# Kernel tuning notes

Measured on AMD Instinct MI355X. Metric: run time of the kernel, lower is better.

## Reference

```python
import jax, jax.numpy as jnp
import numpy as np

N = 50000   # nodes
E = 1600000 # edges
G = 256     # graphs
EPS = 1e-5  # batchnorm eps (torch default)


def _bn(h, g, b):
    # training-mode BatchNorm1d: biased batch stats
    m = h.mean(0)
    v = h.var(0)
    return (h - m) * jax.lax.rsqrt(v + EPS) * g + b


def _mlp(h, W1, b1, g, be, W2, b2):
    # Lin -> BN -> ReLU -> Lin
    h = jax.nn.relu(_bn(h @ W1 + b1, g, be))
    return h @ W2 + b2


def _scatter_mean(v, idx, n):
    s = jax.ops.segment_sum(v, idx, num_segments=n)
    c = jax.ops.segment_sum(jnp.ones((v.shape[0], 1), v.dtype), idx, num_segments=n)
    return s / jnp.maximum(c, 1.0)


def setup_inputs() -> dict:
    key = jax.random.key(0)
    ks = iter(jax.random.split(key, 32))
    d = {}
    d["x"] = jax.random.normal(next(ks), (N, 48), dtype=jnp.float32)
    d["edge_index"] = jax.random.randint(next(ks), (2, E), 0, N, dtype=jnp.int64)
    d["batch"] = jnp.sort(jax.random.randint(next(ks), (N,), 0, G, dtype=jnp.int64))

    def lin(k, fin, fout):
        kw, kb = jax.random.split(k)
        s = 1.0 / np.sqrt(fin)
        return (jax.random.uniform(kw, (fin, fout), jnp.float32, -s, s),
                jax.random.uniform(kb, (fout,), jnp.float32, -s, s))

    # input BatchNorm1d(48)
    d["bn_g"] = jnp.ones((48,), jnp.float32)
    d["bn_b"] = jnp.zeros((48,), jnp.float32)

    def mlp_params(prefix, fin, fmid, fout):
        W1, b1 = lin(next(ks), fin, fmid)
        W2, b2 = lin(next(ks), fmid, fout)
        d[prefix + "_W1"], d[prefix + "_b1"] = W1, b1
        d[prefix + "_g"] = jnp.ones((fmid,), jnp.float32)
        d[prefix + "_be"] = jnp.zeros((fmid,), jnp.float32)
        d[prefix + "_W2"], d[prefix + "_b2"] = W2, b2

    mlp_params("e", 96, 128, 128)    # EdgeBlock
    mlp_params("n1", 176, 128, 128)  # NodeBlock mlp1
    mlp_params("n2", 176, 128, 128)  # NodeBlock mlp2
    mlp_params("gl", 128, 128, 2)    # GlobalBlock
    return d


def reference(x, edge_index, batch, bn_g, bn_b,
              e_W1, e_b1, e_g, e_be, e_W2, e_b2,
              n1_W1, n1_b1, n1_g, n1_be, n1_W2, n1_b2,
              n2_W1, n2_b1, n2_g, n2_be, n2_W2, n2_b2,
              gl_W1, gl_b1, gl_g, gl_be, gl_W2, gl_b2):
    x = _bn(x, bn_g, bn_b)
    row, col = edge_index[0], edge_index[1]
    # EdgeBlock: cat(src, dest) -> MLP
    edge_attr = _mlp(jnp.concatenate([x[row], x[col]], axis=1),
                     e_W1, e_b1, e_g, e_be, e_W2, e_b2)
    # NodeBlock: cat(x[row], edge_attr) -> mlp1 -> scatter_mean(col) -> cat(x,.) -> mlp2
    m = _mlp(jnp.concatenate([x[row], edge_attr], axis=1),
             n1_W1, n1_b1, n1_g, n1_be, n1_W2, n1_b2)
    agg = _scatter_mean(m, col, N)
    x2 = _mlp(jnp.concatenate([x, agg], axis=1),
              n2_W1, n2_b1, n2_g, n2_be, n2_W2, n2_b2)
    # GlobalBlock: scatter_mean over graphs -> MLP -> [G, 2]
    u = _scatter_mean(x2, batch, G)
    u = _mlp(u, gl_W1, gl_b1, gl_g, gl_be, gl_W2, gl_b2)
    return u
```

## Files before the change

kernel.cpp:

```cpp
#include <hip/hip_runtime.h>
#include <hip/hip_bf16.h>
#include <stdint.h>

#define DEV static __device__ __forceinline__

constexpr int N_ = 50000;
constexpr int E_ = 1600000;
constexpr int G_ = 256;

typedef __attribute__((ext_vector_type(8))) short short8;
typedef __attribute__((ext_vector_type(4))) float float4v;

DEV uint16_t f2bf(float f){
  uint32_t u = __float_as_uint(f);
  uint32_t r = (u + 0x7fffu + ((u >> 16) & 1u)) >> 16;
  return (uint16_t)r;
}
DEV void unpack2(uint32_t p, float& a, float& b){
  a = __uint_as_float(p << 16);
  b = __uint_as_float(p & 0xffff0000u);
}
DEV uint32_t pack2(float a, float b){
  return (uint32_t)f2bf(a) | ((uint32_t)f2bf(b) << 16);
}

__global__ __launch_bounds__(256) void k_xstats(const float* __restrict__ x, float* __restrict__ xstats){
  __shared__ float lst[96];
  int t = threadIdx.x;
  if (t < 96) lst[t] = 0.f;
  __syncthreads();
  int gid = blockIdx.x * 256 + t;
  int c4 = (gid % 12) * 4;
  float s[4] = {0,0,0,0}, q[4] = {0,0,0,0};
  const float4v* x4 = (const float4v*)x;
  for (int i = gid; i < N_ * 12; i += 64512){
    float4v v = x4[i];
    #pragma unroll
    for (int j = 0; j < 4; j++){ s[j] += v[j]; q[j] += v[j]*v[j]; }
  }
  #pragma unroll
  for (int j = 0; j < 4; j++){
    atomicAdd(&lst[c4 + j], s[j]);
    atomicAdd(&lst[48 + c4 + j], q[j]);
  }
  __syncthreads();
  if (t < 96) atomicAdd(&xstats[t], lst[t]);
}

__global__ void k_xfin(const float* __restrict__ xstats, const float* __restrict__ g,
                       const float* __restrict__ b, float* __restrict__ sx, float* __restrict__ tx){
  int c = threadIdx.x;
  if (c < 48){
    float m = xstats[c] / (float)N_;
    float v = xstats[48 + c] / (float)N_ - m*m;
    float s = g[c] / sqrtf(v + 1e-5f);
    sx[c] = s; tx[c] = b[c] - m*s;
  }
}

__global__ __launch_bounds__(256) void k_hist(const int* __restrict__ ei, int* __restrict__ counts){
  int e = blockIdx.x * 256 + threadIdx.x;
  if (e < E_) atomicAdd(&counts[ei[E_ + e]], 1);
}

__global__ __launch_bounds__(256) void k_invc(const int* __restrict__ counts, float* __restrict__ invc){
  int n = blockIdx.x * 256 + threadIdx.x;
  if (n < N_){ int c = counts[n]; invc[n] = (c > 0) ? 1.f/(float)c : 0.f; }
}

__global__ __launch_bounds__(256) void k_scan(const int* __restrict__ counts, int* __restrict__ off, int* __restrict__ cur){
  __shared__ int wsum[4];
  __shared__ int carry_s;
  int t = threadIdx.x, lane = t & 63, w = t >> 6;
  if (t == 0) carry_s = 0;
  __syncthreads();
  for (int base = 0; base < N_; base += 1024){
    int i0 = base + t * 4;
    int v0 = (i0 + 0 < N_) ? counts[i0 + 0] : 0;
    int v1 = (i0 + 1 < N_) ? counts[i0 + 1] : 0;
    int v2 = (i0 + 2 < N_) ? counts[i0 + 2] : 0;
    int v3 = (i0 + 3 < N_) ? counts[i0 + 3] : 0;
    int tsum = v0 + v1 + v2 + v3;
    int xs = tsum;
    for (int d = 1; d < 64; d <<= 1){ int y = __shfl_up(xs, d); if (lane >= d) xs += y; }
    if (lane == 63) wsum[w] = xs;
    __syncthreads();
    int woff = 0;
    for (int k = 0; k < w; k++) woff += wsum[k];
    int excl = xs - tsum + woff + carry_s;
    int e0 = excl, e1 = e0 + v0, e2 = e1 + v1, e3 = e2 + v2;
    if (i0 + 0 < N_){ off[i0+0] = e0; cur[i0+0] = e0; }
    if (i0 + 1 < N_){ off[i0+1] = e1; cur[i0+1] = e1; }
    if (i0 + 2 < N_){ off[i0+2] = e2; cur[i0+2] = e2; }
    if (i0 + 3 < N_){ off[i0+3] = e3; cur[i0+3] = e3; }
    __syncthreads();
    if (t == 0) carry_s += wsum[0] + wsum[1] + wsum[2] + wsum[3];
    __syncthreads();
  }
  if (t == 0) off[N_] = carry_s;
}

__global__ __launch_bounds__(256) void k_place(const int* __restrict__ ei, int* __restrict__ cur,
                                               int2* __restrict__ rcs){
  int e = blockIdx.x * 256 + threadIdx.x;
  if (e < E_){
    int c = ei[E_ + e];
    int p = atomicAdd(&cur[c], 1);
    rcs[p] = make_int2(ei[e], c);
  }
}

__global__ __launch_bounds__(256) void k_wprep(
    const float* __restrict__ eW2, const float* __restrict__ n1W1,
    const float* __restrict__ n1W2, const float* __restrict__ n2W1,
    const float* __restrict__ n2W2, const float* __restrict__ glW1,
    const float* __restrict__ n1b2, const float* __restrict__ n2b2,
    uint16_t* __restrict__ Mt, float* __restrict__ Wcomb,
    float* __restrict__ M3, float* __restrict__ c1, float* __restrict__ c3){
  int flat = blockIdx.x * 256 + threadIdx.x;
  if (flat < 16384){
    int n = flat & 127, k = flat >> 7;
    float a = 0.f;
    for (int j = 0; j < 128; j++) a += eW2[k*128 + j] * n1W1[(48 + j)*128 + n];
    Mt[n*128 + k] = f2bf(a);
  } else if (flat < 32768){
    int b = flat - 16384;
    int n = b & 127, j = b >> 7;
    float a = 0.f;
    for (int m = 0; m < 128; m++) a += n1W2[j*128 + m] * n2W1[(48 + m)*128 + n];
    Wcomb[(48 + j)*128 + n] = a;
  } else if (flat < 38912){
    int b = flat - 32768;
    int n = b & 127, k = b >> 7;
    Wcomb[k*128 + n] = n2W1[k*128 + n];
  } else if (flat < 55296){
    int b = flat - 38912;
    int n = b & 127, j = b >> 7;
    float a = 0.f;
    for (int m = 0; m < 128; m++) a += n2W2[j*128 + m] * glW1[m*128 + n];
    M3[j*128 + n] = a;
  } else if (flat < 55552){
    int e = flat - 55296;
    if (e < 128){
      float a = 0.f;
      for (int m = 0; m < 128; m++) a += n1b2[m] * n2W1[(48 + m)*128 + e];
      c1[e] = a;
    } else {
      int n = e - 128;
      float a = 0.f;
      for (int m = 0; m < 128; m++) a += n2b2[m] * glW1[m*128 + n];
      c3[n] = a;
    }
  }
}

__global__ __launch_bounds__(256) void k_nodegemm(
    const float* __restrict__ x, const float* __restrict__ sx, const float* __restrict__ tx,
    const float* __restrict__ eW1, const float* __restrict__ n1W1,
    uint16_t* __restrict__ AC, uint16_t* __restrict__ Bn){
  __shared__ float xT[48][36];
  __shared__ float W[48][128];
  int t = threadIdx.x;
  int n0 = blockIdx.x * 32;
  for (int idx = t; idx < 384; idx += 256){
    int r = idx / 12, q = idx % 12;
    int n = n0 + r;
    float4v v = {0.f,0.f,0.f,0.f};
    if (n < N_) v = *(const float4v*)&x[(size_t)n*48 + q*4];
    #pragma unroll
    for (int i = 0; i < 4; i++){
      int k = q*4 + i;
      xT[k][r] = v[i] * sx[k] + tx[k];
    }
  }
  int cg = t & 31, ng = t >> 5;
  const float* Wsrc0 = eW1;
  const float* Wsrc1 = eW1 + 48*128;
  const float* Wsrc2 = n1W1;
  for (int seg = 0; seg < 3; seg++){
    const float* Wsrc = (seg == 0) ? Wsrc0 : (seg == 1) ? Wsrc1 : Wsrc2;
    __syncthreads();
    {
      const float4v* src4 = (const float4v*)Wsrc;
      float4v* W4 = (float4v*)W;
      for (int idx = t; idx < 1536; idx += 256) W4[idx] = src4[idx];
    }
    __syncthreads();
    float acc[4][4] = {{0.f}};
    #pragma unroll 4
    for (int k = 0; k < 48; k++){
      float4v xv = *(const float4v*)&xT[k][ng*4];
      float4v wv = *(const float4v*)&W[k][cg*4];
      #pragma unroll
      for (int i = 0; i < 4; i++)
        #pragma unroll
        for (int j = 0; j < 4; j++)
          acc[i][j] += xv[i]*wv[j];
    }
    #pragma unroll
    for (int i = 0; i < 4; i++){
      int n = n0 + ng*4 + i;
      if (n >= N_) continue;
      uint2 pv;
      pv.x = pack2(acc[i][0], acc[i][1]);
      pv.y = pack2(acc[i][2], acc[i][3]);
      if (seg == 0)      *(uint2*)&AC[(size_t)n*256 + cg*4] = pv;
      else if (seg == 1) *(uint2*)&Bn[(size_t)n*128 + cg*4] = pv;
      else               *(uint2*)&AC[(size_t)n*256 + 128 + cg*4] = pv;
    }
  }
}

__global__ __launch_bounds__(256) void k_estats(const int2* __restrict__ rcs,
    const uint16_t* __restrict__ AC, const uint16_t* __restrict__ Bn, float* __restrict__ estR){
  __shared__ float red[4][64][4];
  __shared__ float lst[256];
  int t = threadIdx.x, lane = t & 63, w = t >> 6;
  int wid = blockIdx.x * 4 + w, nw = gridDim.x * 4;
  float s0=0,q0=0,s1=0,q1=0;
  const uint32_t* ACu = (const uint32_t*)AC;
  const uint32_t* Bu  = (const uint32_t*)Bn;
  for (int e = wid; e < E_; e += nw){
    int2 rc = rcs[e];
    uint32_t pa = ACu[(size_t)rc.x*128 + lane];
    uint32_t pb = Bu[(size_t)rc.y*64 + lane];
    float a0,a1,b0,b1; unpack2(pa,a0,a1); unpack2(pb,b0,b1);
    float h0 = a0 + b0, h1 = a1 + b1;
    s0 += h0; q0 += h0*h0; s1 += h1; q1 += h1*h1;
  }
  red[w][lane][0]=s0; red[w][lane][1]=q0; red[w][lane][2]=s1; red[w][lane][3]=q1;
  __syncthreads();
  if (t < 64){
    float S0=0,Q0=0,S1=0,Q1=0;
    for (int ww = 0; ww < 4; ww++){ S0+=red[ww][t][0]; Q0+=red[ww][t][1]; S1+=red[ww][t][2]; Q1+=red[ww][t][3]; }
    lst[2*t] = S0; lst[2*t+1] = S1; lst[128+2*t] = Q0; lst[128+2*t+1] = Q1;
  }
  __syncthreads();
  atomicAdd(&estR[(blockIdx.x & 63)*256 + t], lst[t]);
}

__global__ void k_bnfin(const float* __restrict__ statsR, int reps, const float* __restrict__ g,
                        const float* __restrict__ be, float* __restrict__ s_out, float* __restrict__ t_out,
                        float inv_n){
  int c = threadIdx.x;
  if (c >= 128) return;
  float sm = 0.f, sq = 0.f;
  for (int r = 0; r < reps; r++){ sm += statsR[r*256 + c]; sq += statsR[r*256 + 128 + c]; }
  float m = sm * inv_n;
  float v = sq * inv_n - m*m;
  float s = g[c] / sqrtf(v + 1e-5f);
  s_out[c] = s;
  t_out[c] = be[c] - m*s;
}

__global__ __launch_bounds__(256) void k_epass(
    const int2* __restrict__ rcs,
    const uint16_t* __restrict__ AC, const uint16_t* __restrict__ Bn,
    const uint16_t* __restrict__ Mt, const float* __restrict__ se, const float* __restrict__ te,
    const float* __restrict__ sn1, const float* __restrict__ tn1,
    int mode, float* __restrict__ n1R, float* __restrict__ aggf){
  __shared__ __align__(16) uint16_t bufA[64*136];
  __shared__ __align__(16) uint16_t bufB[128*136];
  __shared__ float sete[512];
  __shared__ float lst[256];
  __shared__ int srow[64], scol[64], ssid[64], scolseg[64];
  __shared__ int snseg;
  const int t = threadIdx.x;
  const long i0 = (long)blockIdx.x * 64;
  const int lane = t & 63, w = t >> 6;
  const int m = lane & 15, quad = lane >> 4;

  if (t < 128){ sete[t] = se[t]; sete[128 + t] = te[t]; sete[256 + t] = sn1[t]; sete[384 + t] = tn1[t]; }
  if (mode == 0) lst[t] = 0.f;
  if (t < 64){ int2 rc = rcs[i0 + t]; srow[t] = rc.x; scol[t] = rc.y; }
  __syncthreads();

  if (mode == 1 && t < 64){
    bool bnd = (t > 0) && (scol[t] != scol[t-1]);
    unsigned long long mask = __ballot(bnd);
    int sid = __popcll(mask << (63 - t));
    ssid[t] = sid;
    if (bnd || t == 0) scolseg[sid] = scol[t];
    if (t == 63) snseg = sid + 1;
  }

  {
    int e = t >> 2, q = t & 3;
    int r = srow[e], c = scol[e];
    const uint4* Ap = (const uint4*)((const uint32_t*)AC + (size_t)r*128 + q*16);
    const uint4* Bp = (const uint4*)((const uint32_t*)Bn + (size_t)c*64  + q*16);
    uint4* dst = (uint4*)((uint32_t*)bufA + e*68 + q*16);
    int cb = q*32;
    #pragma unroll
    for (int u = 0; u < 4; u++){
      uint4 va = Ap[u], vb = Bp[u];
      float4v sA = *(const float4v*)&sete[cb + u*8];
      float4v sB = *(const float4v*)&sete[cb + u*8 + 4];
      float4v tA = *(const float4v*)&sete[128 + cb + u*8];
      float4v tB = *(const float4v*)&sete[128 + cb + u*8 + 4];
      float a0,a1,b0,b1; uint4 o;
      unpack2(va.x,a0,a1); unpack2(vb.x,b0,b1);
      o.x = pack2(fmaxf(0.f,(a0+b0)*sA[0]+tA[0]), fmaxf(0.f,(a1+b1)*sA[1]+tA[1]));
      unpack2(va.y,a0,a1); unpack2(vb.y,b0,b1);
      o.y = pack2(fmaxf(0.f,(a0+b0)*sA[2]+tA[2]), fmaxf(0.f,(a1+b1)*sA[3]+tA[3]));
      unpack2(va.z,a0,a1); unpack2(vb.z,b0,b1);
      o.z = pack2(fmaxf(0.f,(a0+b0)*sB[0]+tB[0]), fmaxf(0.f,(a1+b1)*sB[1]+tB[1]));
      unpack2(va.w,a0,a1); unpack2(vb.w,b0,b1);
      o.w = pack2(fmaxf(0.f,(a0+b0)*sB[2]+tB[2]), fmaxf(0.f,(a1+b1)*sB[3]+tB[3]));
      dst[u] = o;
    }
  }
  {
    int n = t >> 1, h = t & 1;
    const uint4* src = (const uint4*)((const uint32_t*)Mt + n*64 + h*32);
    uint4* dst = (uint4*)((uint32_t*)bufB + n*68 + h*32);
    #pragma unroll
    for (int u = 0; u < 8; u++) dst[u] = src[u];
  }
  __syncthreads();

  float4v acc[8];
  #pragma unroll
  for (int nt = 0; nt < 8; nt++){ acc[nt][0]=0.f; acc[nt][1]=0.f; acc[nt][2]=0.f; acc[nt][3]=0.f; }
  {
    const uint16_t* aptr = bufA + (w*16 + m)*136 + quad*8;
    const uint16_t* bbase = bufB + m*136 + quad*8;
    #pragma unroll
    for (int ks = 0; ks < 4; ks++){
      short8 af = *(const short8*)(aptr + ks*32);
      #pragma unroll
      for (int nt = 0; nt < 8; nt++){
        short8 bf = *(const short8*)(bbase + nt*16*136 + ks*32);
        acc[nt] = __builtin_amdgcn_mfma_f32_16x16x32_bf16(af, bf, acc[nt], 0, 0, 0);
      }
    }
  }
  __syncthreads();

  {
    int e = t >> 2, q = t & 3;
    int r = srow[e];
    const uint4* src = (const uint4*)((const uint32_t*)AC + (size_t)r*128 + 64 + q*16);
    uint4* dst = (uint4*)((uint32_t*)bufA + e*68 + q*16);
    #pragma unroll
    for (int u = 0; u < 4; u++) dst[u] = src[u];
  }
  #pragma unroll
  for (int nt = 0; nt < 8; nt++)
    #pragma unroll
    for (int reg = 0; reg < 4; reg++)
      bufB[(w*16 + quad*4 + reg)*136 + nt*16 + m] = f2bf(acc[nt][reg]);
  if (mode == 1 && snseg <= 32){
    float* segacc = (float*)(bufB + 8704);
    for (int i = t; i < snseg*128; i += 256) segacc[i] = 0.f;
  }
  __syncthreads();

  if (mode == 0){
    int cp = t & 63, eg = t >> 6;
    float ss0=0,qq0=0,ss1=0,qq1=0;
    #pragma unroll
    for (int it = 0; it < 16; it++){
      int e = eg*16 + it;
      uint32_t ph = ((uint32_t*)bufB)[e*68 + cp];
      uint32_t pc = ((uint32_t*)bufA)[e*68 + cp];
      float h0,h1,c0,c1v;
      unpack2(ph,h0,h1); unpack2(pc,c0,c1v);
      float v0 = h0 + c0, v1 = h1 + c1v;
      ss0 += v0; qq0 += v0*v0; ss1 += v1; qq1 += v1*v1;
    }
    atomicAdd(&lst[2*cp], ss0);
    atomicAdd(&lst[2*cp+1], ss1);
    atomicAdd(&lst[128+2*cp], qq0);
    atomicAdd(&lst[128+2*cp+1], qq1);
    __syncthreads();
    atomicAdd(&n1R[(blockIdx.x & 63)*256 + t], lst[t]);
  } else {
    int cp = t & 63, eg = t >> 6;
    float s0 = sete[256+2*cp], s1 = sete[256+2*cp+1];
    float b0 = sete[384+2*cp], b1 = sete[384+2*cp+1];
    int nseg = snseg;
    bool lp = (nseg <= 32);
    float* segacc = (float*)(bufB + 8704);
    int cursid = ssid[eg*16];
    float r0 = 0.f, r1 = 0.f;
    for (int it = 0; it < 16; it++){
      int e = eg*16 + it;
      uint32_t ph = ((uint32_t*)bufB)[e*68 + cp];
      uint32_t pc = ((uint32_t*)bufA)[e*68 + cp];
      float h0,h1,c0,c1v;
      unpack2(ph,h0,h1); unpack2(pc,c0,c1v);
      float v0 = fmaxf(0.f, (h0+c0)*s0 + b0);
      float v1 = fmaxf(0.f, (h1+c1v)*s1 + b1);
      int sid = ssid[e];
      if (sid != cursid){
        if (lp){ atomicAdd(&segacc[cursid*128 + 2*cp], r0); atomicAdd(&segacc[cursid*128 + 2*cp+1], r1); }
        else { int c = scolseg[cursid];
               atomicAdd(&aggf[(size_t)c*128 + 2*cp], r0); atomicAdd(&aggf[(size_t)c*128 + 2*cp+1], r1); }
        cursid = sid; r0 = 0.f; r1 = 0.f;
      }
      r0 += v0; r1 += v1;
    }
    if (lp){ atomicAdd(&segacc[cursid*128 + 2*cp], r0); atomicAdd(&segacc[cursid*128 + 2*cp+1], r1); }
    else { int c = scolseg[cursid];
           atomicAdd(&aggf[(size_t)c*128 + 2*cp], r0); atomicAdd(&aggf[(size_t)c*128 + 2*cp+1], r1); }
    __syncthreads();
    if (lp){
      for (int idx = t; idx < nseg*64; idx += 256){
        int s = idx >> 6, cpp = idx & 63;
        float v0 = segacc[s*128 + 2*cpp], v1 = segacc[s*128 + 2*cpp+1];
        int c = scolseg[s];
        float* dst = &aggf[(size_t)c*128 + 2*cpp];
        if (s == 0 || s == nseg - 1){ atomicAdd(dst, v0); atomicAdd(dst+1, v1); }
        else { dst[0] = v0; dst[1] = v1; }
      }
    }
  }
}

__global__ __launch_bounds__(256) void k_n2(const float* __restrict__ x,
    const float* __restrict__ sx, const float* __restrict__ tx,
    const float* __restrict__ aggf, const float* __restrict__ invc,
    const float* __restrict__ Wc, const float* __restrict__ c1, const int* __restrict__ counts,
    float* __restrict__ hn2, float* __restrict__ n2R){
  __shared__ float xT[44][36];
  __shared__ float wT[44][128];
  __shared__ float lst[256];
  int t = threadIdx.x;
  int n0 = blockIdx.x * 32;
  int cg = t & 31, ng = t >> 5;
  lst[t] = 0.f;
  float acc[4][4] = {{0.f}};
  for (int kc = 0; kc < 176; kc += 44){
    __syncthreads();
    for (int idx = t; idx < 32*44; idx += 256){
      int r = idx / 44, k = idx % 44;
      int n = n0 + r, kk = kc + k;
      float v = 0.f;
      if (n < N_){
        if (kk < 48) v = x[(size_t)n*48 + kk] * sx[kk] + tx[kk];
        else         v = aggf[(size_t)n*128 + (kk - 48)] * invc[n];
      }
      xT[k][r] = v;
    }
    for (int idx = t; idx < 44*128; idx += 256){
      int k = idx >> 7, c = idx & 127;
      wT[k][c] = Wc[(kc + k)*128 + c];
    }
    __syncthreads();
    for (int k = 0; k < 44; k++){
      float4v xv = *(const float4v*)&xT[k][ng*4];
      float4v wv = *(const float4v*)&wT[k][cg*4];
      #pragma unroll
      for (int i = 0; i < 4; i++)
        #pragma unroll
        for (int j = 0; j < 4; j++)
          acc[i][j] += xv[i]*wv[j];
    }
  }
  float csum[4] = {0,0,0,0}, cqs[4] = {0,0,0,0};
  for (int i = 0; i < 4; i++){
    int n = n0 + ng*4 + i;
    if (n >= N_) continue;
    bool ok = counts[n] > 0;
    float4v o;
    #pragma unroll
    for (int j = 0; j < 4; j++){
      float vv = acc[i][j] + (ok ? c1[cg*4 + j] : 0.f);
      o[j] = vv; csum[j] += vv; cqs[j] += vv*vv;
    }
    *(float4v*)&hn2[(size_t)n*128 + cg*4] = o;
  }
  #pragma unroll
  for (int j = 0; j < 4; j++){
    atomicAdd(&lst[cg*4 + j], csum[j]);
    atomicAdd(&lst[128 + cg*4 + j], cqs[j]);
  }
  __syncthreads();
  atomicAdd(&n2R[(blockIdx.x & 63)*256 + t], lst[t]);
}

__global__ void k_goff(const int* __restrict__ batch, int* __restrict__ goff){
  int g = threadIdx.x;
  int lo = 0, hi = N_;
  while (lo < hi){ int mid = (lo + hi) >> 1; if (batch[mid] < g) lo = mid + 1; else hi = mid; }
  goff[g] = lo;
  if (g == 0) goff[256] = N_;
}

__global__ __launch_bounds__(128) void k_gmean(const float* __restrict__ hn2, const int* __restrict__ goff,
    const float* __restrict__ sn2, const float* __restrict__ tn2, float* __restrict__ gmean){
  int g = blockIdx.x, c = threadIdx.x;
  int b = goff[g], e = goff[g+1];
  float s = sn2[c], tt = tn2[c], a = 0.f;
  for (int r = b; r < e; r++) a += fmaxf(0.f, hn2[(size_t)r*128 + c]*s + tt);
  gmean[g*128 + c] = (e > b) ? a/(float)(e - b) : 0.f;
}

__global__ __launch_bounds__(256) void k_hg(const float* __restrict__ gmean, const float* __restrict__ M3,
    const float* __restrict__ c3, const int* __restrict__ goff,
    float* __restrict__ hg, float* __restrict__ gls){
  int idx = blockIdx.x * 256 + threadIdx.x;
  int g = idx >> 7, c = idx & 127;
  float a = 0.f;
  for (int k = 0; k < 128; k++) a += gmean[g*128 + k] * M3[k*128 + c];
  if (goff[g+1] > goff[g]) a += c3[c];
  hg[idx] = a;
  atomicAdd(&gls[c], a);
  atomicAdd(&gls[128 + c], a*a);
}

__global__ __launch_bounds__(256) void k_out(const float* __restrict__ hg, const float* __restrict__ sgl,
    const float* __restrict__ tgl, const float* __restrict__ glW2, const float* __restrict__ glb2,
    float* __restrict__ out){
  int idx = blockIdx.x * 256 + threadIdx.x;
  int g = idx >> 1, o = idx & 1;
  float a = 0.f;
  for (int c = 0; c < 128; c++){
    float r = fmaxf(0.f, hg[g*128 + c]*sgl[c] + tgl[c]);
    a += r * glW2[c*2 + o];
  }
  out[idx] = a + glb2[o];
}

extern "C" void kernel_launch(void* const* d_in, const int* in_sizes, int n_in,
                              void* d_out, int out_size, void* d_ws, size_t ws_size,
                              hipStream_t stream){
  const float* x     = (const float*)d_in[0];
  const int*   ei    = (const int*)d_in[1];
  const int*   batch = (const int*)d_in[2];
  const float* bn_g  = (const float*)d_in[3];
  const float* bn_b  = (const float*)d_in[4];
  const float* eW1   = (const float*)d_in[5];
  const float* e_g   = (const float*)d_in[7];
  const float* e_be  = (const float*)d_in[8];
  const float* eW2   = (const float*)d_in[9];
  const float* n1W1  = (const float*)d_in[11];
  const float* n1_g  = (const float*)d_in[13];
  const float* n1_be = (const float*)d_in[14];
  const float* n1W2  = (const float*)d_in[15];
  const float* n1b2  = (const float*)d_in[16];
  const float* n2W1  = (const float*)d_in[17];
  const float* n2_g  = (const float*)d_in[19];
  const float* n2_be = (const float*)d_in[20];
  const float* n2W2  = (const float*)d_in[21];
  const float* n2b2  = (const float*)d_in[22];
  const float* glW1  = (const float*)d_in[23];
  const float* gl_g  = (const float*)d_in[25];
  const float* gl_be = (const float*)d_in[26];
  const float* glW2  = (const float*)d_in[27];
  const float* glb2  = (const float*)d_in[28];
  float* out = (float*)d_out;

  char* w = (char*)d_ws;
  size_t off = 0;
  auto take = [&](size_t bytes) -> char* {
    char* p = w + off;
    off = (off + bytes + 511) & ~(size_t)511;
    return p;
  };

  const size_t ZONE_WORDS = 96 + 3*64*256 + 256 + N_;
  float* zone   = (float*)take(ZONE_WORDS * 4);
  float* xstats = zone;
  float* estR   = zone + 96;
  float* n1R    = zone + 96 + 64*256;
  float* n2R    = zone + 96 + 2*64*256;
  float* gls    = zone + 96 + 3*64*256;
  int*   counts = (int*)(zone + 96 + 3*64*256 + 256);

  float* sx = (float*)take(48*4);   float* tx = (float*)take(48*4);
  float* se = (float*)take(128*4);  float* te = (float*)take(128*4);
  float* sn1 = (float*)take(128*4); float* tn1 = (float*)take(128*4);
  float* sn2 = (float*)take(128*4); float* tn2 = (float*)take(128*4);
  float* sgl = (float*)take(128*4); float* tgl = (float*)take(128*4);
  float* c1 = (float*)take(128*4);  float* c3 = (float*)take(128*4);
  float* invc  = (float*)take((size_t)N_*4);
  float* Wcomb = (float*)take(176*128*4);
  float* M3    = (float*)take(128*128*4);
  float* gmean = (float*)take(G_*128*4);
  float* hg    = (float*)take(G_*128*4);
  int* offs = (int*)take((N_+1)*4);
  int* cur  = (int*)take(N_*4);
  int* goff = (int*)take(257*4);
  uint16_t* Mt = (uint16_t*)take(128*128*2);
  uint16_t* AC = (uint16_t*)take((size_t)N_*256*2);
  uint16_t* Bn = (uint16_t*)take((size_t)N_*128*2);
  float* aggf  = (float*)take((size_t)N_*128*4);
  float* hn2   = (float*)take((size_t)N_*128*4);
  int2* rcs = (int2*)take((size_t)E_*8);

  if (off > ws_size) return;

  hipMemsetAsync(zone, 0, ZONE_WORDS*4, stream);
  hipMemsetAsync(aggf, 0, (size_t)N_*128*4, stream);

  hipLaunchKernelGGL(k_xstats, dim3(252), dim3(256), 0, stream, x, xstats);
  hipLaunchKernelGGL(k_hist, dim3((E_+255)/256), dim3(256), 0, stream, ei, counts);
  hipLaunchKernelGGL(k_xfin, dim3(1), dim3(64), 0, stream, xstats, bn_g, bn_b, sx, tx);
  hipLaunchKernelGGL(k_scan, dim3(1), dim3(256), 0, stream, counts, offs, cur);
  hipLaunchKernelGGL(k_place, dim3((E_+255)/256), dim3(256), 0, stream, ei, cur, rcs);
  hipLaunchKernelGGL(k_invc, dim3((N_+255)/256), dim3(256), 0, stream, counts, invc);
  hipLaunchKernelGGL(k_wprep, dim3(217), dim3(256), 0, stream,
                     eW2, n1W1, n1W2, n2W1, n2W2, glW1, n1b2, n2b2, Mt, Wcomb, M3, c1, c3);
  hipLaunchKernelGGL(k_nodegemm, dim3((N_+31)/32), dim3(256), 0, stream,
                     x, sx, tx, eW1, n1W1, AC, Bn);
  hipLaunchKernelGGL(k_estats, dim3(1024), dim3(256), 0, stream, rcs, AC, Bn, estR);
  hipLaunchKernelGGL(k_bnfin, dim3(1), dim3(128), 0, stream, estR, 64, e_g, e_be, se, te, 1.f/(float)E_);
  hipLaunchKernelGGL(k_epass, dim3(E_/64), dim3(256), 0, stream,
                     rcs, AC, Bn, Mt, se, te, se, te, 0, n1R, aggf);
  hipLaunchKernelGGL(k_bnfin, dim3(1), dim3(128), 0, stream, n1R, 64, n1_g, n1_be, sn1, tn1, 1.f/(float)E_);
  hipLaunchKernelGGL(k_epass, dim3(E_/64), dim3(256), 0, stream,
                     rcs, AC, Bn, Mt, se, te, sn1, tn1, 1, n1R, aggf);
  hipLaunchKernelGGL(k_n2, dim3((N_+31)/32), dim3(256), 0, stream,
                     x, sx, tx, aggf, invc, Wcomb, c1, counts, hn2, n2R);
  hipLaunchKernelGGL(k_bnfin, dim3(1), dim3(128), 0, stream, n2R, 64, n2_g, n2_be, sn2, tn2, 1.f/(float)N_);
  hipLaunchKernelGGL(k_goff, dim3(1), dim3(256), 0, stream, batch, goff);
  hipLaunchKernelGGL(k_gmean, dim3(256), dim3(128), 0, stream, hn2, goff, sn2, tn2, gmean);
  hipLaunchKernelGGL(k_hg, dim3(128), dim3(256), 0, stream, gmean, M3, c3, goff, hg, gls);
  hipLaunchKernelGGL(k_bnfin, dim3(1), dim3(128), 0, stream, gls, 1, gl_g, gl_be, sgl, tgl, 1.f/(float)G_);
  hipLaunchKernelGGL(k_out, dim3(2), dim3(256), 0, stream, hg, sgl, tgl, glW2, glb2, out);
}
```

Baseline: 1.691 ms.

## Split edge pass into stats and aggregate kernels with smaller LDS footprint

Replaces the mode-switched edge-pass kernel with two specialised kernels. The stats kernel computes BN sums straight from MFMA accumulators with wave shuffles, so it no longer writes the bf16 hidden tile back to LDS. Both kernels shrink the LDS row pitch from 136 to 132 and pack segment and scale scratch into the B buffer, cutting shared memory per block to fit more blocks per CU. The trade-off is a smaller segment-accumulator limit (24 instead of 32), which sends more blocks to global atomics, plus a changed bank-conflict pattern from the new padding.

```diff
diff --git a/kernel.cpp b/kernel.cpp
--- a/kernel.cpp
+++ b/kernel.cpp
@@ -16,6 +16,7 @@
   uint32_t r = (u + 0x7fffu + ((u >> 16) & 1u)) >> 16;
   return (uint16_t)r;
 }
+DEV float bf2f(uint16_t v){ return __uint_as_float((uint32_t)v << 16); }
 DEV void unpack2(uint32_t p, float& a, float& b){
   a = __uint_as_float(p << 16);
   b = __uint_as_float(p & 0xffff0000u);
@@ -253,43 +254,32 @@
   t_out[c] = be[c] - m*s;
 }
 
-__global__ __launch_bounds__(256) void k_epass(
+__global__ __launch_bounds__(256) void k_epass0(
     const int2* __restrict__ rcs,
     const uint16_t* __restrict__ AC, const uint16_t* __restrict__ Bn,
     const uint16_t* __restrict__ Mt, const float* __restrict__ se, const float* __restrict__ te,
-    const float* __restrict__ sn1, const float* __restrict__ tn1,
-    int mode, float* __restrict__ n1R, float* __restrict__ aggf){
-  __shared__ __align__(16) uint16_t bufA[64*136];
-  __shared__ __align__(16) uint16_t bufB[128*136];
-  __shared__ float sete[512];
+    float* __restrict__ n1R){
+  __shared__ __align__(16) uint16_t bufA[64*132];
+  __shared__ __align__(16) uint16_t bufB[128*132];
+  __shared__ float sete[256];
   __shared__ float lst[256];
-  __shared__ int srow[64], scol[64], ssid[64], scolseg[64];
-  __shared__ int snseg;
+  __shared__ int srow[64], scol[64];
   const int t = threadIdx.x;
   const long i0 = (long)blockIdx.x * 64;
   const int lane = t & 63, w = t >> 6;
   const int m = lane & 15, quad = lane >> 4;
 
-  if (t < 128){ sete[t] = se[t]; sete[128 + t] = te[t]; sete[256 + t] = sn1[t]; sete[384 + t] = tn1[t]; }
-  if (mode == 0) lst[t] = 0.f;
+  if (t < 128){ sete[t] = se[t]; sete[128 + t] = te[t]; }
+  lst[t] = 0.f;
   if (t < 64){ int2 rc = rcs[i0 + t]; srow[t] = rc.x; scol[t] = rc.y; }
   __syncthreads();
-
-  if (mode == 1 && t < 64){
-    bool bnd = (t > 0) && (scol[t] != scol[t-1]);
-    unsigned long long mask = __ballot(bnd);
-    int sid = __popcll(mask << (63 - t));
-    ssid[t] = sid;
-    if (bnd || t == 0) scolseg[sid] = scol[t];
-    if (t == 63) snseg = sid + 1;
-  }
 
   {
     int e = t >> 2, q = t & 3;
     int r = srow[e], c = scol[e];
     const uint4* Ap = (const uint4*)((const uint32_t*)AC + (size_t)r*128 + q*16);
     const uint4* Bp = (const uint4*)((const uint32_t*)Bn + (size_t)c*64  + q*16);
-    uint4* dst = (uint4*)((uint32_t*)bufA + e*68 + q*16);
+    uint4* dst = (uint4*)((uint32_t*)bufA + e*66 + q*16);
     int cb = q*32;
     #pragma unroll
     for (int u = 0; u < 4; u++){
@@ -313,7 +303,7 @@
   {
     int n = t >> 1, h = t & 1;
     const uint4* src = (const uint4*)((const uint32_t*)Mt + n*64 + h*32);
-    uint4* dst = (uint4*)((uint32_t*)bufB + n*68 + h*32);
+    uint4* dst = (uint4*)((uint32_t*)bufB + n*66 + h*32);
     #pragma unroll
     for (int u = 0; u < 8; u++) dst[u] = src[u];
   }
@@ -323,14 +313,14 @@
   #pragma unroll
   for (int nt = 0; nt < 8; nt++){ acc[nt][0]=0.f; acc[nt][1]=0.f; acc[nt][2]=0.f; acc[nt][3]=0.f; }
   {
-    const uint16_t* aptr = bufA + (w*16 + m)*136 + quad*8;
-    const uint16_t* bbase = bufB + m*136 + quad*8;
+    const uint16_t* aptr = bufA + (w*16 + m)*132 + quad*8;
+    const uint16_t* bbase = bufB + m*132 + quad*8;
     #pragma unroll
     for (int ks = 0; ks < 4; ks++){
       short8 af = *(const short8*)(aptr + ks*32);
       #pragma unroll
       for (int nt = 0; nt < 8; nt++){
-        short8 bf = *(const short8*)(bbase + nt*16*136 + ks*32);
+        short8 bf = *(const short8*)(bbase + nt*16*132 + ks*32);
         acc[nt] = __builtin_amdgcn_mfma_f32_16x16x32_bf16(af, bf, acc[nt], 0, 0, 0);
       }
     }
@@ -341,7 +331,118 @@
     int e = t >> 2, q = t & 3;
     int r = srow[e];
     const uint4* src = (const uint4*)((const uint32_t*)AC + (size_t)r*128 + 64 + q*16);
-    uint4* dst = (uint4*)((uint32_t*)bufA + e*68 + q*16);
+    uint4* dst = (uint4*)((uint32_t*)bufA + e*66 + q*16);
+    #pragma unroll
+    for (int u = 0; u < 4; u++) dst[u] = src[u];
+  }
+  __syncthreads();
+
+  #pragma unroll
+  for (int nt = 0; nt < 8; nt++){
+    float ss = 0.f, qq = 0.f;
+    #pragma unroll
+    for (int reg = 0; reg < 4; reg++){
+      int e = w*16 + quad*4 + reg;
+      float cv = bf2f(bufA[e*132 + nt*16 + m]);
+      float h = acc[nt][reg] + cv;
+      ss += h; qq += h*h;
+    }
+    ss += __shfl_xor(ss, 16); ss += __shfl_xor(ss, 32);
+    qq += __shfl_xor(qq, 16); qq += __shfl_xor(qq, 32);
+    if (quad == 0){
+      atomicAdd(&lst[nt*16 + m], ss);
+      atomicAdd(&lst[128 + nt*16 + m], qq);
+    }
+  }
+  __syncthreads();
+  atomicAdd(&n1R[(blockIdx.x & 63)*256 + t], lst[t]);
+}
+
+__global__ __launch_bounds__(256) void k_epass1(
+    const int2* __restrict__ rcs,
+    const uint16_t* __restrict__ AC, const uint16_t* __restrict__ Bn,
+    const uint16_t* __restrict__ Mt, const float* __restrict__ se, const float* __restrict__ te,
+    const float* __restrict__ sn1, const float* __restrict__ tn1,
+    float* __restrict__ aggf){
+  __shared__ __align__(16) uint16_t bufA[64*132];
+  __shared__ __align__(16) uint16_t bufB[128*132];
+  __shared__ float sete[256];
+  __shared__ int srow[64], scol[64];
+  __shared__ int snseg;
+  const int t = threadIdx.x;
+  const long i0 = (long)blockIdx.x * 64;
+  const int lane = t & 63, w = t >> 6;
+  const int m = lane & 15, quad = lane >> 4;
+
+  uint32_t* bufBu = (uint32_t*)bufB;
+  float* segacc  = (float*)(bufBu + 4224);
+  float* sn1c    = (float*)(bufBu + 7296);
+  float* tn1c    = (float*)(bufBu + 7424);
+  int*   ssid_s  = (int*)(bufBu + 7552);
+  int*   scseg_s = (int*)(bufBu + 7616);
+
+  if (t < 128){ sete[t] = se[t]; sete[128 + t] = te[t]; }
+  if (t < 64){ int2 rc = rcs[i0 + t]; srow[t] = rc.x; scol[t] = rc.y; }
+  __syncthreads();
+
+  {
+    int e = t >> 2, q = t & 3;
+    int r = srow[e], c = scol[e];
+    const uint4* Ap = (const uint4*)((const uint32_t*)AC + (size_t)r*128 + q*16);
+    const uint4* Bp = (const uint4*)((const uint32_t*)Bn + (size_t)c*64  + q*16);
+    uint4* dst = (uint4*)((uint32_t*)bufA + e*66 + q*16);
+    int cb = q*32;
+    #pragma unroll
+    for (int u = 0; u < 4; u++){
+      uint4 va = Ap[u], vb = Bp[u];
+      float4v sA = *(const float4v*)&sete[cb + u*8];
+      float4v sB = *(const float4v*)&sete[cb + u*8 + 4];
+      float4v tA = *(const float4v*)&sete[128 + cb + u*8];
+      float4v tB = *(const float4v*)&sete[128 + cb + u*8 + 4];
+      float a0,a1,b0,b1; uint4 o;
+      unpack2(va.x,a0,a1); unpack2(vb.x,b0,b1);
+      o.x = pack2(fmaxf(0.f,(a0+b0)*sA[0]+tA[0]), fmaxf(0.f,(a1+b1)*sA[1]+tA[1]));
+      unpack2(va.y,a0,a1); unpack2(vb.y,b0,b1);
+      o.y = pack2(fmaxf(0.f,(a0+b0)*sA[2]+tA[2]), fmaxf(0.f,(a1+b1)*sA[3]+tA[3]));
+      unpack2(va.z,a0,a1); unpack2(vb.z,b0,b1);
+      o.z = pack2(fmaxf(0.f,(a0+b0)*sB[0]+tB[0]), fmaxf(0.f,(a1+b1)*sB[1]+tB[1]));
+      unpack2(va.w,a0,a1); unpack2(vb.w,b0,b1);
+      o.w = pack2(fmaxf(0.f,(a0+b0)*sB[2]+tB[2]), fmaxf(0.f,(a1+b1)*sB[3]+tB[3]));
+      dst[u] = o;
+    }
+  }
+  {
+    int n = t >> 1, h = t & 1;
+    const uint4* src = (const uint4*)((const uint32_t*)Mt + n*64 + h*32);
+    uint4* dst = (uint4*)((uint32_t*)bufB + n*66 + h*32);
+    #pragma unroll
+    for (int u = 0; u < 8; u++) dst[u] = src[u];
+  }
+  __syncthreads();
+
+  float4v acc[8];
+  #pragma unroll
+  for (int nt = 0; nt < 8; nt++){ acc[nt][0]=0.f; acc[nt][1]=0.f; acc[nt][2]=0.f; acc[nt][3]=0.f; }
+  {
+    const uint16_t* aptr = bufA + (w*16 + m)*132 + quad*8;
+    const uint16_t* bbase = bufB + m*132 + quad*8;
+    #pragma unroll
+    for (int ks = 0; ks < 4; ks++){
+      short8 af = *(const short8*)(aptr + ks*32);
+      #pragma unroll
+      for (int nt = 0; nt < 8; nt++){
+        short8 bf = *(const short8*)(bbase + nt*16*132 + ks*32);
+        acc[nt] = __builtin_amdgcn_mfma_f32_16x16x32_bf16(af, bf, acc[nt], 0, 0, 0);
+      }
+    }
+  }
+  __syncthreads();
+
+  {
+    int e = t >> 2, q = t & 3;
+    int r = srow[e];
+    const uint4* src = (const uint4*)((const uint32_t*)AC + (size_t)r*128 + 64 + q*16);
+    uint4* dst = (uint4*)((uint32_t*)bufA + e*66 + q*16);
     #pragma unroll
     for (int u = 0; u < 4; u++) dst[u] = src[u];
   }
@@ -349,67 +450,55 @@
   for (int nt = 0; nt < 8; nt++)
     #pragma unroll
     for (int reg = 0; reg < 4; reg++)
-      bufB[(w*16 + quad*4 + reg)*136 + nt*16 + m] = f2bf(acc[nt][reg]);
-  if (mode == 1 && snseg <= 32){
-    float* segacc = (float*)(bufB + 8704);
-    for (int i = t; i < snseg*128; i += 256) segacc[i] = 0.f;
-  }
-  __syncthreads();
-
-  if (mode == 0){
+      bufB[(w*16 + quad*4 + reg)*132 + nt*16 + m] = f2bf(acc[nt][reg]);
+  if (t < 64){
+    bool bnd = (t > 0) && (scol[t] != scol[t-1]);
+    unsigned long long mask = __ballot(bnd);
+    int sid = __popcll(mask << (63 - t));
+    ssid_s[t] = sid;
+    if (bnd || t == 0) scseg_s[sid] = scol[t];
+    if (t == 63) snseg = sid + 1;
+  } else if (t < 192){
+    int c = t - 64;
+    sn1c[c] = sn1[c]; tn1c[c] = tn1[c];
+  }
+  for (int i = t; i < 24*128; i += 256) segacc[i] = 0.f;
+  __syncthreads();
+
+  {
     int cp = t & 63, eg = t >> 6;
-    float ss0=0,qq0=0,ss1=0,qq1=0;
-    #pragma unroll
-    for (int it = 0; it < 16; it++){
-      int e = eg*16 + it;
-      uint32_t ph = ((uint32_t*)bufB)[e*68 + cp];
-      uint32_t pc = ((uint32_t*)bufA)[e*68 + cp];
-      float h0,h1,c0,c1v;
-      unpack2(ph,h0,h1); unpack2(pc,c0,c1v);
-      float v0 = h0 + c0, v1 = h1 + c1v;
-      ss0 += v0; qq0 += v0*v0; ss1 += v1; qq1 += v1*v1;
-    }
-    atomicAdd(&lst[2*cp], ss0);
-    atomicAdd(&lst[2*cp+1], ss1);
-    atomicAdd(&lst[128+2*cp], qq0);
-    atomicAdd(&lst[128+2*cp+1], qq1);
-    __syncthreads();
-    atomicAdd(&n1R[(blockIdx.x & 63)*256 + t], lst[t]);
-  } else {
-    int cp = t & 63, eg = t >> 6;
-    float s0 = sete[256+2*cp], s1 = sete[256+2*cp+1];
-    float b0 = sete[384+2*cp], b1 = sete[384+2*cp+1];
+    float s0 = sn1c[2*cp], s1 = sn1c[2*cp+1];
+    float b0 = tn1c[2*cp], b1 = tn1c[2*cp+1];
     int nseg = snseg;
-    bool lp = (nseg <= 32);
-    float* segacc = (float*)(bufB + 8704);
-    int cursid = ssid[eg*16];
+    bool lp = (nseg <= 24);
+    int cursid = ssid_s[eg*16];
     float r0 = 0.f, r1 = 0.f;
     for (int it = 0; it < 16; it++){
       int e = eg*16 + it;
-      uint32_t ph = ((uint32_t*)bufB)[e*68 + cp];
-      uint32_t pc = ((uint32_t*)bufA)[e*68 + cp];
+      uint32_t ph = bufBu[e*66 + cp];
+      uint32_t pc = ((uint32_t*)bufA)[e*66 + cp];
       float h0,h1,c0,c1v;
       unpack2(ph,h0,h1); unpack2(pc,c0,c1v);
       float v0 = fmaxf(0.f, (h0+c0)*s0 + b0);
       float v1 = fmaxf(0.f, (h1+c1v)*s1 + b1);
-      int sid = ssid[e];
+      int sid = ssid_s[e];
       if (sid != cursid){
         if (lp){ atomicAdd(&segacc[cursid*128 + 2*cp], r0); atomicAdd(&segacc[cursid*128 + 2*cp+1], r1); }
-        else { int c = scolseg[cursid];
+        else { int c = scseg_s[cursid];
                atomicAdd(&aggf[(size_t)c*128 + 2*cp], r0); atomicAdd(&aggf[(size_t)c*128 + 2*cp+1], r1); }
         cursid = sid; r0 = 0.f; r1 = 0.f;
       }
       r0 += v0; r1 += v1;
     }
     if (lp){ atomicAdd(&segacc[cursid*128 + 2*cp], r0); atomicAdd(&segacc[cursid*128 + 2*cp+1], r1); }
-    else { int c = scolseg[cursid];
+    else { int c = scseg_s[cursid];
            atomicAdd(&aggf[(size_t)c*128 + 2*cp], r0); atomicAdd(&aggf[(size_t)c*128 + 2*cp+1], r1); }
     __syncthreads();
     if (lp){
       for (int idx = t; idx < nseg*64; idx += 256){
         int s = idx >> 6, cpp = idx & 63;
         float v0 = segacc[s*128 + 2*cpp], v1 = segacc[s*128 + 2*cpp+1];
-        int c = scolseg[s];
+        int c = scseg_s[s];
         float* dst = &aggf[(size_t)c*128 + 2*cpp];
         if (s == 0 || s == nseg - 1){ atomicAdd(dst, v0); atomicAdd(dst+1, v1); }
         else { dst[0] = v0; dst[1] = v1; }
@@ -607,11 +696,11 @@
                      x, sx, tx, eW1, n1W1, AC, Bn);
   hipLaunchKernelGGL(k_estats, dim3(1024), dim3(256), 0, stream, rcs, AC, Bn, estR);
   hipLaunchKernelGGL(k_bnfin, dim3(1), dim3(128), 0, stream, estR, 64, e_g, e_be, se, te, 1.f/(float)E_);
-  hipLaunchKernelGGL(k_epass, dim3(E_/64), dim3(256), 0, stream,
-                     rcs, AC, Bn, Mt, se, te, se, te, 0, n1R, aggf);
+  hipLaunchKernelGGL(k_epass0, dim3(E_/64), dim3(256), 0, stream,
+                     rcs, AC, Bn, Mt, se, te, n1R);
   hipLaunchKernelGGL(k_bnfin, dim3(1), dim3(128), 0, stream, n1R, 64, n1_g, n1_be, sn1, tn1, 1.f/(float)E_);
-  hipLaunchKernelGGL(k_epass, dim3(E_/64), dim3(256), 0, stream,
-                     rcs, AC, Bn, Mt, se, te, sn1, tn1, 1, n1R, aggf);
+  hipLaunchKernelGGL(k_epass1, dim3(E_/64), dim3(256), 0, stream,
+                     rcs, AC, Bn, Mt, se, te, sn1, tn1, aggf);
   hipLaunchKernelGGL(k_n2, dim3((N_+31)/32), dim3(256), 0, stream,
                      x, sx, tx, aggf, invc, Wcomb, c1, counts, hn2, n2R);
   hipLaunchKernelGGL(k_bnfin, dim3(1), dim3(128), 0, stream, n2R, 64, n2_g, n2_be, sn2, tn2, 1.f/(float)N_);
```

New measurement: 2.351 ms. 39.1% more time.
